# Optimization experiments

Measured on AMD Instinct MI355X. Metric: run time of the kernel, lower is better.

## Reference

```python
import jax, jax.numpy as jnp
import numpy as np

N = 250000   # num nodes
E = 250000   # num edges (tree: ~one parent per node)
D = 128      # embed_size
H = 256      # MLP hidden
HOPS = 3


def _mlp(x, w1, b1, w2, b2):
    # Sequential(Linear, ReLU, Linear, ReLU, Dropout(eval=identity))
    return jax.nn.relu(jnp.dot(jax.nn.relu(jnp.dot(x, w1) + b1), w2) + b2)


def _scatter_mean(src, idx, n):
    s = jax.ops.segment_sum(src, idx, num_segments=n)
    c = jax.ops.segment_sum(jnp.ones((src.shape[0],), src.dtype), idx, num_segments=n)
    return s / jnp.maximum(c, 1.0)[:, None]


def setup_inputs() -> dict:
    key = jax.random.key(0)
    ks = jax.random.split(key, 32)
    u = lambda k, shp: jax.random.uniform(k, shp, jnp.float32, -0.1, 0.1)
    inp = {
        "batch_token": jax.random.normal(ks[0], (N, D), jnp.float32),
        "self_idx_batch": jax.random.randint(ks[1], (E,), 0, N),
        "parent_idx_batch": jax.random.randint(ks[2], (E,), 0, N),
        "root_mask": (jax.random.uniform(ks[3], (N,)) < 0.01).astype(jnp.float32),
        "leaf_mask": (jax.random.uniform(ks[4], (N,)) < 0.3).astype(jnp.float32),
        "start_token": jax.random.normal(ks[5], (D,), jnp.float32),
        "end_token": jax.random.normal(ks[6], (D,), jnp.float32),
        # MLP_V: D -> H -> D
        "Vw1": u(ks[7], (D, H)), "Vb1": u(ks[8], (H,)), "Vw2": u(ks[9], (H, D)), "Vb2": u(ks[10], (D,)),
        # MLP_E: 1 -> H -> D
        "Ew1": u(ks[11], (1, H)), "Eb1": u(ks[12], (H,)), "Ew2": u(ks[13], (H, D)), "Eb2": u(ks[14], (D,)),
        # MLP_p: 3D -> H -> D
        "Pw1": u(ks[15], (3 * D, H)), "Pb1": u(ks[16], (H,)), "Pw2": u(ks[17], (H, D)), "Pb2": u(ks[18], (D,)),
        # MLP_c: 3D -> H -> D
        "Cw1": u(ks[19], (3 * D, H)), "Cb1": u(ks[20], (H,)), "Cw2": u(ks[21], (H, D)), "Cb2": u(ks[22], (D,)),
        # MLP_aggr: 3D -> H -> D
        "Aw1": u(ks[23], (3 * D, H)), "Ab1": u(ks[24], (H,)), "Aw2": u(ks[25], (H, D)), "Ab2": u(ks[26], (D,)),
    }
    return inp


def reference(batch_token, self_idx_batch, parent_idx_batch, root_mask, leaf_mask,
              start_token, end_token,
              Vw1, Vb1, Vw2, Vb2,
              Ew1, Eb1, Ew2, Eb2,
              Pw1, Pb1, Pw2, Pb2,
              Cw1, Cb1, Cw2, Cb2,
              Aw1, Ab1, Aw2, Ab2):
    n = batch_token.shape[0]
    edge_in = _mlp(jnp.ones((1, 1), batch_token.dtype), Ew1, Eb1, Ew2, Eb2)   # [1,D]
    edge_out = _mlp(jnp.zeros((1, 1), batch_token.dtype), Ew1, Eb1, Ew2, Eb2)  # [1,D]
    e = self_idx_batch.shape[0]
    edge_in = jnp.broadcast_to(edge_in, (e, edge_in.shape[1]))
    edge_out = jnp.broadcast_to(edge_out, (e, edge_out.shape[1]))

    hidden = _mlp(batch_token, Vw1, Vb1, Vw2, Vb2)  # [N,D]
    for _ in range(HOPS):
        node_self = hidden[self_idx_batch]      # [E,D] gather
        node_parent = hidden[parent_idx_batch]  # [E,D] gather
        inp_parent = jnp.concatenate([node_parent, node_self, edge_out], axis=-1)  # [E,3D]
        inp_child = jnp.concatenate([node_self, node_parent, edge_in], axis=-1)    # [E,3D]
        S_p = _mlp(inp_parent, Pw1, Pb1, Pw2, Pb2)
        S_c = _mlp(inp_child, Cw1, Cb1, Cw2, Cb2)
        S_p = _scatter_mean(S_p, self_idx_batch, n)
        S_c = _scatter_mean(S_c, parent_idx_batch, n)
        S_p = S_p + root_mask[:, None] * start_token
        S_c = S_c + leaf_mask[:, None] * end_token
        x_aggr = jnp.concatenate([hidden, S_p, S_c], axis=-1)  # [N,3D]
        hidden = hidden + _mlp(x_aggr, Aw1, Ab1, Aw2, Ab2)
    return hidden
```

## Files before the change

### kernel.cpp

```cpp
#include <hip/hip_runtime.h>

typedef __attribute__((ext_vector_type(8))) short short8;
typedef __attribute__((ext_vector_type(4))) float f32x4;

#define DD 128
#define HH 256

__device__ __forceinline__ unsigned short f2bf(float f) {
  unsigned int u = __float_as_uint(f);
  u += 0x7fffu + ((u >> 16) & 1u);
  return (unsigned short)(u >> 16);
}
__device__ __forceinline__ float bf2f(unsigned short s) {
  return __uint_as_float(((unsigned int)s) << 16);
}
__device__ __forceinline__ f32x4 mfma16(short8 a, short8 b, f32x4 c) {
  return __builtin_amdgcn_mfma_f32_16x16x32_bf16(a, b, c, 0, 0, 0);
}

__global__ void wconv(const float* __restrict__ src, unsigned short* __restrict__ dst,
                      int K, int Nout, int kswap) {
  int id = blockIdx.x * 256 + threadIdx.x;
  if (id >= K * Nout) return;
  int n = id / K, k = id - n * K;
  int ks = k + kswap; if (ks >= K) ks -= K;
  dst[n * K + k] = f2bf(src[(size_t)ks * Nout + n]);
}

__global__ void prep_bias(const float* __restrict__ Ew1, const float* __restrict__ Eb1,
                          const float* __restrict__ Ew2, const float* __restrict__ Eb2,
                          const float* __restrict__ Pw1, const float* __restrict__ Pb1,
                          const float* __restrict__ Cw1, const float* __restrict__ Cb1,
                          float* __restrict__ b1P, float* __restrict__ b1C) {
  __shared__ float h1[HH], h0[HH], ein[DD], eout[DD];
  int t = threadIdx.x;
  h1[t] = fmaxf(Ew1[t] + Eb1[t], 0.f);
  h0[t] = fmaxf(Eb1[t], 0.f);
  __syncthreads();
  if (t < DD) {
    float s1 = Eb2[t], s0 = Eb2[t];
    for (int j = 0; j < HH; ++j) { s1 += h1[j] * Ew2[j * DD + t]; s0 += h0[j] * Ew2[j * DD + t]; }
    ein[t]  = fmaxf(s1, 0.f);
    eout[t] = fmaxf(s0, 0.f);
  }
  __syncthreads();
  float bp = Pb1[t], bc = Cb1[t];
  for (int d = 0; d < DD; ++d) {
    bp += eout[d] * Pw1[(size_t)(256 + d) * HH + t];
    bc += ein[d]  * Cw1[(size_t)(256 + d) * HH + t];
  }
  b1P[t] = bp; b1C[t] = bc;
}

__global__ void count_k(const int* __restrict__ selfI, const int* __restrict__ parI,
                        int* degP, int* degC, int E) {
  int id = blockIdx.x * 256 + threadIdx.x;
  if (id < E) { atomicAdd(&degP[selfI[id]], 1); atomicAdd(&degC[parI[id]], 1); }
}

__global__ void scan1(const int* __restrict__ src, int* __restrict__ dst,
                      int* __restrict__ part, int n) {
  __shared__ int sh[256];
  int t = threadIdx.x;
  int base = blockIdx.x * 1024 + t * 4;
  int v0 = base + 0 < n ? src[base + 0] : 0;
  int v1 = base + 1 < n ? src[base + 1] : 0;
  int v2 = base + 2 < n ? src[base + 2] : 0;
  int v3 = base + 3 < n ? src[base + 3] : 0;
  int tsum = v0 + v1 + v2 + v3;
  sh[t] = tsum;
  __syncthreads();
  for (int off = 1; off < 256; off <<= 1) {
    int y = (t >= off) ? sh[t - off] : 0;
    __syncthreads();
    if (t >= off) sh[t] += y;
    __syncthreads();
  }
  int ex = sh[t] - tsum;
  if (base + 0 < n) dst[base + 0] = ex;
  if (base + 1 < n) dst[base + 1] = ex + v0;
  if (base + 2 < n) dst[base + 2] = ex + v0 + v1;
  if (base + 3 < n) dst[base + 3] = ex + v0 + v1 + v2;
  if (t == 255) part[blockIdx.x] = sh[255];
}

__global__ void scan2(int* __restrict__ part, int m) {
  __shared__ int sh[256];
  int t = threadIdx.x;
  int carry = 0;
  for (int base = 0; base < m; base += 256) {
    int v = (base + t < m) ? part[base + t] : 0;
    sh[t] = v;
    __syncthreads();
    for (int off = 1; off < 256; off <<= 1) {
      int y = (t >= off) ? sh[t - off] : 0;
      __syncthreads();
      if (t >= off) sh[t] += y;
      __syncthreads();
    }
    if (base + t < m) part[base + t] = carry + sh[t] - v;
    int tot = sh[255];
    __syncthreads();
    carry += tot;
  }
}

__global__ void scan3(int* __restrict__ dst, const int* __restrict__ part, int n) {
  int i = blockIdx.x * 256 + threadIdx.x;
  if (i < n) dst[i] += part[i >> 10];
}

__global__ void copy2(const int* __restrict__ a, int* __restrict__ b,
                      const int* __restrict__ c, int* __restrict__ d, int n) {
  int i = blockIdx.x * 256 + threadIdx.x;
  if (i < n) { b[i] = a[i]; d[i] = c[i]; }
}

__global__ void pos_k(const int* __restrict__ selfI, const int* __restrict__ parI,
                      int* curP, int* curC, int* posP, int* posC, int E) {
  int e = blockIdx.x * 256 + threadIdx.x;
  if (e < E) {
    posP[e] = atomicAdd(&curP[selfI[e]], 1);
    posC[e] = atomicAdd(&curC[parI[e]], 1);
  }
}

__global__ __launch_bounds__(256) void v_kernel(
    const float* __restrict__ x, const unsigned short* __restrict__ W1t,
    const unsigned short* __restrict__ W2t, const float* __restrict__ b1,
    const float* __restrict__ b2, float* __restrict__ hidden, int n) {
  __shared__ __align__(16) unsigned short A[64 * 136];
  __shared__ __align__(16) unsigned short O1[64 * 264];
  int t = threadIdx.x;
  int w = t >> 6, lane = t & 63, ln = lane & 15, quad = lane >> 4, qo = quad * 8;
  long tile0 = (long)blockIdx.x * 64;
  int rl = t >> 2, part = t & 3;
  long gr = tile0 + rl;
  const float* src = x + (size_t)(gr < n ? gr : 0) * DD + part * 32;
  unsigned short* arow = A + rl * 136 + part * 32;
#pragma unroll
  for (int i = 0; i < 8; ++i) {
    float4 v = *(const float4*)(src + i * 4);
    *(ushort4*)(arow + i * 4) = make_ushort4(f2bf(v.x), f2bf(v.y), f2bf(v.z), f2bf(v.w));
  }
  const unsigned short* aRow = A + (w * 16 + ln) * 136;
  f32x4 zero4 = {0.f, 0.f, 0.f, 0.f};
  f32x4 acc1[16];
#pragma unroll
  for (int nt = 0; nt < 16; ++nt) acc1[nt] = zero4;
#pragma unroll
  for (int kt = 0; kt < 4; ++kt) {
    short8 a = *(const short8*)(aRow + kt * 32 + qo);
#pragma unroll
    for (int nt = 0; nt < 16; ++nt) {
      short8 b = *(const short8*)(W1t + (size_t)(nt * 16 + ln) * 128 + kt * 32 + qo);
      acc1[nt] = mfma16(a, b, acc1[nt]);
    }
  }
#pragma unroll
  for (int nt = 0; nt < 16; ++nt) {
    float bb = b1[nt * 16 + ln];
#pragma unroll
    for (int r = 0; r < 4; ++r)
      O1[(w * 16 + quad * 4 + r) * 264 + nt * 16 + ln] = f2bf(fmaxf(acc1[nt][r] + bb, 0.f));
  }
  const unsigned short* oRow = O1 + (w * 16 + ln) * 264;
  f32x4 acc2[8];
#pragma unroll
  for (int nt = 0; nt < 8; ++nt) acc2[nt] = zero4;
#pragma unroll
  for (int kt = 0; kt < 8; ++kt) {
    short8 a = *(const short8*)(oRow + kt * 32 + qo);
#pragma unroll
    for (int nt = 0; nt < 8; ++nt) {
      short8 b = *(const short8*)(W2t + (size_t)(nt * 16 + ln) * 256 + kt * 32 + qo);
      acc2[nt] = mfma16(a, b, acc2[nt]);
    }
  }
#pragma unroll
  for (int nt = 0; nt < 8; ++nt) {
    float bb = b2[nt * 16 + ln];
#pragma unroll
    for (int r = 0; r < 4; ++r) {
      long gr2 = tile0 + w * 16 + quad * 4 + r;
      if (gr2 < n) hidden[gr2 * DD + nt * 16 + ln] = fmaxf(acc2[nt][r] + bb, 0.f);
    }
  }
}

__global__ __launch_bounds__(512, 4) void edge_kernel(
    const float* __restrict__ hidden, const int* __restrict__ selfI, const int* __restrict__ parI,
    const int* __restrict__ posP, const int* __restrict__ posC,
    const unsigned short* __restrict__ Pw1t, const unsigned short* __restrict__ Pw2t,
    const unsigned short* __restrict__ Cw1t, const unsigned short* __restrict__ Cw2t,
    const float* __restrict__ b1P, const float* __restrict__ b1C,
    const float* __restrict__ b2P, const float* __restrict__ b2C,
    unsigned short* __restrict__ SpE, unsigned short* __restrict__ ScE, int E) {
  __shared__ __align__(16) unsigned short A[64 * 264];
  __shared__ __align__(16) unsigned short O1[64 * 264];
  int t = threadIdx.x;
  int w = t >> 6, lane = t & 63, ln = lane & 15, quad = lane >> 4, qo = quad * 8;
  long tile0 = (long)blockIdx.x * 64;
  int rl = t >> 3, part = t & 7;
  long ge = tile0 + rl;
  bool vrow = ge < E;
  int si = vrow ? selfI[ge] : 0;
  int pi = vrow ? parI[ge] : 0;
  const float* src = (part < 4) ? (hidden + (size_t)si * DD + part * 32)
                                : (hidden + (size_t)pi * DD + (part - 4) * 32);
  unsigned short* dstA = A + rl * 264 + part * 32;
#pragma unroll
  for (int i = 0; i < 8; ++i) {
    float4 v = *(const float4*)(src + i * 4);
    *(ushort4*)(dstA + i * 4) = make_ushort4(f2bf(v.x), f2bf(v.y), f2bf(v.z), f2bf(v.w));
  }
  __syncthreads();

  for (int mlp = 0; mlp < 2; ++mlp) {
    const unsigned short* W1t = mlp ? Cw1t : Pw1t;
    const unsigned short* W2t = mlp ? Cw2t : Pw2t;
    const float* b1 = mlp ? b1C : b1P;
    const float* b2 = mlp ? b2C : b2P;
    unsigned short* Sout = mlp ? ScE : SpE;
    const int* pos = mlp ? posC : posP;
    f32x4 acc[4][2];
#pragma unroll
    for (int m = 0; m < 4; ++m) {
      acc[m][0] = {0.f, 0.f, 0.f, 0.f}; acc[m][1] = {0.f, 0.f, 0.f, 0.f};
    }
#pragma unroll
    for (int kt = 0; kt < 8; ++kt) {
      short8 a[4];
#pragma unroll
      for (int m = 0; m < 4; ++m)
        a[m] = *(const short8*)(A + (m * 16 + ln) * 264 + kt * 32 + qo);
#pragma unroll
      for (int nn = 0; nn < 2; ++nn) {
        short8 b = *(const short8*)(W1t + (size_t)(w * 32 + nn * 16 + ln) * 256 + kt * 32 + qo);
#pragma unroll
        for (int m = 0; m < 4; ++m) acc[m][nn] = mfma16(a[m], b, acc[m][nn]);
      }
    }
#pragma unroll
    for (int nn = 0; nn < 2; ++nn) {
      int col = w * 32 + nn * 16 + ln;
      float bb = b1[col];
#pragma unroll
      for (int m = 0; m < 4; ++m)
#pragma unroll
        for (int r = 0; r < 4; ++r)
          O1[(m * 16 + quad * 4 + r) * 264 + col] = f2bf(fmaxf(acc[m][nn][r] + bb, 0.f));
    }
    __syncthreads();
    f32x4 acc2[4];
#pragma unroll
    for (int m = 0; m < 4; ++m) acc2[m] = {0.f, 0.f, 0.f, 0.f};
#pragma unroll
    for (int kt = 0; kt < 8; ++kt) {
      short8 b = *(const short8*)(W2t + (size_t)(w * 16 + ln) * 256 + kt * 32 + qo);
#pragma unroll
      for (int m = 0; m < 4; ++m) {
        short8 a = *(const short8*)(O1 + (m * 16 + ln) * 264 + kt * 32 + qo);
        acc2[m] = mfma16(a, b, acc2[m]);
      }
    }
    __syncthreads();
    {
      int col = w * 16 + ln;
      float bb = b2[col];
#pragma unroll
      for (int m = 0; m < 4; ++m)
#pragma unroll
        for (int r = 0; r < 4; ++r)
          O1[(m * 16 + quad * 4 + r) * 264 + col] = f2bf(fmaxf(acc2[m][r] + bb, 0.f));
    }
    __syncthreads();
    if (vrow) {
      int dpos = pos[ge];
      const unsigned short* srow = O1 + rl * 264 + part * 16;
      ushort4* dst = (ushort4*)(Sout + (size_t)dpos * DD + part * 16);
#pragma unroll
      for (int i = 0; i < 4; ++i) dst[i] = *(const ushort4*)(srow + i * 4);
    }
    __syncthreads();
  }
}

__global__ __launch_bounds__(512, 4) void node_kernel(
    float* __restrict__ hidden,
    const unsigned short* __restrict__ SpE, const unsigned short* __restrict__ ScE,
    const int* __restrict__ offP, const int* __restrict__ degP,
    const int* __restrict__ offC, const int* __restrict__ degC,
    const float* __restrict__ rootM, const float* __restrict__ leafM,
    const float* __restrict__ startT, const float* __restrict__ endT,
    const unsigned short* __restrict__ W1t, const unsigned short* __restrict__ W2t,
    const float* __restrict__ b1, const float* __restrict__ b2, int n) {
  __shared__ __align__(16) unsigned short A[64 * 392];
  int t = threadIdx.x;
  int w = t >> 6, lane = t & 63, ln = lane & 15, quad = lane >> 4, qo = quad * 8;
  long tile0 = (long)blockIdx.x * 64;
  int rl = t >> 3, part = t & 7;
  int c0 = part * 16;
  long gr = tile0 + rl;
  long g = (gr < n) ? gr : 0;
  unsigned short* arow = A + rl * 392;
  {
    const float* hrow = hidden + (size_t)g * DD + c0;
#pragma unroll
    for (int i = 0; i < 4; ++i) {
      float4 h = *(const float4*)(hrow + i * 4);
      *(ushort4*)(arow + c0 + i * 4) = make_ushort4(f2bf(h.x), f2bf(h.y), f2bf(h.z), f2bf(h.w));
    }
  }
  {
    int off = offP[g], dg = degP[g];
    float s[16];
#pragma unroll
    for (int i = 0; i < 16; ++i) s[i] = 0.f;
    for (int j = 0; j < dg; ++j) {
      const unsigned short* rr = SpE + (size_t)(off + j) * DD + c0;
#pragma unroll
      for (int i = 0; i < 4; ++i) {
        ushort4 u = *(const ushort4*)(rr + i * 4);
        s[i * 4 + 0] += bf2f(u.x); s[i * 4 + 1] += bf2f(u.y);
        s[i * 4 + 2] += bf2f(u.z); s[i * 4 + 3] += bf2f(u.w);
      }
    }
    float ip = 1.f / fmaxf((float)dg, 1.f);
    float rm = rootM[g];
#pragma unroll
    for (int i = 0; i < 4; ++i) {
      float4 st = *(const float4*)(startT + c0 + i * 4);
      *(ushort4*)(arow + 128 + c0 + i * 4) = make_ushort4(
          f2bf(s[i * 4 + 0] * ip + rm * st.x), f2bf(s[i * 4 + 1] * ip + rm * st.y),
          f2bf(s[i * 4 + 2] * ip + rm * st.z), f2bf(s[i * 4 + 3] * ip + rm * st.w));
    }
  }
  {
    int off = offC[g], dg = degC[g];
    float s[16];
#pragma unroll
    for (int i = 0; i < 16; ++i) s[i] = 0.f;
    for (int j = 0; j < dg; ++j) {
      const unsigned short* rr = ScE + (size_t)(off + j) * DD + c0;
#pragma unroll
      for (int i = 0; i < 4; ++i) {
        ushort4 u = *(const ushort4*)(rr + i * 4);
        s[i * 4 + 0] += bf2f(u.x); s[i * 4 + 1] += bf2f(u.y);
        s[i * 4 + 2] += bf2f(u.z); s[i * 4 + 3] += bf2f(u.w);
      }
    }
    float ic = 1.f / fmaxf((float)dg, 1.f);
    float lm = leafM[g];
#pragma unroll
    for (int i = 0; i < 4; ++i) {
      float4 et = *(const float4*)(endT + c0 + i * 4);
      *(ushort4*)(arow + 256 + c0 + i * 4) = make_ushort4(
          f2bf(s[i * 4 + 0] * ic + lm * et.x), f2bf(s[i * 4 + 1] * ic + lm * et.y),
          f2bf(s[i * 4 + 2] * ic + lm * et.z), f2bf(s[i * 4 + 3] * ic + lm * et.w));
    }
  }
  __syncthreads();
  f32x4 acc[4][2];
#pragma unroll
  for (int m = 0; m < 4; ++m) {
    acc[m][0] = {0.f, 0.f, 0.f, 0.f}; acc[m][1] = {0.f, 0.f, 0.f, 0.f};
  }
#pragma unroll
  for (int kt = 0; kt < 12; ++kt) {
    short8 a[4];
#pragma unroll
    for (int m = 0; m < 4; ++m)
      a[m] = *(const short8*)(A + (m * 16 + ln) * 392 + kt * 32 + qo);
#pragma unroll
    for (int nn = 0; nn < 2; ++nn) {
      short8 b = *(const short8*)(W1t + (size_t)(w * 32 + nn * 16 + ln) * 384 + kt * 32 + qo);
#pragma unroll
      for (int m = 0; m < 4; ++m) acc[m][nn] = mfma16(a[m], b, acc[m][nn]);
    }
  }
  __syncthreads();
#pragma unroll
  for (int nn = 0; nn < 2; ++nn) {
    int col = w * 32 + nn * 16 + ln;
    float bb = b1[col];
#pragma unroll
    for (int m = 0; m < 4; ++m)
#pragma unroll
      for (int r = 0; r < 4; ++r)
        A[(m * 16 + quad * 4 + r) * 392 + col] = f2bf(fmaxf(acc[m][nn][r] + bb, 0.f));
  }
  __syncthreads();
  f32x4 acc2[4];
#pragma unroll
  for (int m = 0; m < 4; ++m) acc2[m] = {0.f, 0.f, 0.f, 0.f};
#pragma unroll
  for (int kt = 0; kt < 8; ++kt) {
    short8 b = *(const short8*)(W2t + (size_t)(w * 16 + ln) * 256 + kt * 32 + qo);
#pragma unroll
    for (int m = 0; m < 4; ++m) {
      short8 a = *(const short8*)(A + (m * 16 + ln) * 392 + kt * 32 + qo);
      acc2[m] = mfma16(a, b, acc2[m]);
    }
  }
  __syncthreads();
  {
    int col = w * 16 + ln;
    float bb = b2[col];
#pragma unroll
    for (int m = 0; m < 4; ++m)
#pragma unroll
      for (int r = 0; r < 4; ++r)
        ((float*)(A + (size_t)(m * 16 + quad * 4 + r) * 392))[col] =
            fmaxf(acc2[m][r] + bb, 0.f);
  }
  __syncthreads();
  if (gr < n) {
    const float* F = (const float*)(A + (size_t)rl * 392);
    float* hrow = hidden + (size_t)gr * DD + c0;
#pragma unroll
    for (int i = 0; i < 4; ++i) {
      float4 v = *(const float4*)(F + c0 + i * 4);
      float4 h = *(const float4*)(hrow + i * 4);
      h.x += v.x; h.y += v.y; h.z += v.z; h.w += v.w;
      *(float4*)(hrow + i * 4) = h;
    }
  }
}

extern "C" void kernel_launch(void* const* d_in, const int* in_sizes, int n_in,
                              void* d_out, int out_size, void* d_ws, size_t ws_size,
                              hipStream_t stream) {
  const float* batch  = (const float*)d_in[0];
  const int*   selfI  = (const int*)d_in[1];
  const int*   parI   = (const int*)d_in[2];
  const float* rootM  = (const float*)d_in[3];
  const float* leafM  = (const float*)d_in[4];
  const float* startT = (const float*)d_in[5];
  const float* endT   = (const float*)d_in[6];
  const float* Vw1 = (const float*)d_in[7],  *Vb1 = (const float*)d_in[8];
  const float* Vw2 = (const float*)d_in[9],  *Vb2 = (const float*)d_in[10];
  const float* Ew1 = (const float*)d_in[11], *Eb1 = (const float*)d_in[12];
  const float* Ew2 = (const float*)d_in[13], *Eb2 = (const float*)d_in[14];
  const float* Pw1 = (const float*)d_in[15], *Pb1 = (const float*)d_in[16];
  const float* Pw2 = (const float*)d_in[17], *Pb2 = (const float*)d_in[18];
  const float* Cw1 = (const float*)d_in[19], *Cb1 = (const float*)d_in[20];
  const float* Cw2 = (const float*)d_in[21], *Cb2 = (const float*)d_in[22];
  const float* Aw1 = (const float*)d_in[23], *Ab1 = (const float*)d_in[24];
  const float* Aw2 = (const float*)d_in[25], *Ab2 = (const float*)d_in[26];

  const int N = in_sizes[3];
  const int E = in_sizes[1];
  float* out = (float*)d_out;

  char* p = (char*)d_ws;
  auto nxt = [&](size_t sz) { char* r = p; p += (sz + 255) & ~(size_t)255; return r; };
  unsigned short* SpE = (unsigned short*)nxt((size_t)E * DD * 2);
  unsigned short* ScE = (unsigned short*)nxt((size_t)E * DD * 2);
  int* degP = (int*)nxt((size_t)N * 4);
  int* degC = (int*)nxt((size_t)N * 4);
  int* offP = (int*)nxt((size_t)N * 4);
  int* offC = (int*)nxt((size_t)N * 4);
  int* curP = (int*)nxt((size_t)N * 4);
  int* curC = (int*)nxt((size_t)N * 4);
  int* posP = (int*)nxt((size_t)E * 4);
  int* posC = (int*)nxt((size_t)E * 4);
  int* partA = (int*)nxt(4096);
  int* partB = (int*)nxt(4096);
  unsigned short* Vw1t = (unsigned short*)nxt((size_t)128 * 256 * 2);
  unsigned short* Vw2t = (unsigned short*)nxt((size_t)256 * 128 * 2);
  unsigned short* Pw1t = (unsigned short*)nxt((size_t)256 * 256 * 2);
  unsigned short* Pw2t = (unsigned short*)nxt((size_t)256 * 128 * 2);
  unsigned short* Cw1t = (unsigned short*)nxt((size_t)256 * 256 * 2);
  unsigned short* Cw2t = (unsigned short*)nxt((size_t)256 * 128 * 2);
  unsigned short* Aw1t = (unsigned short*)nxt((size_t)384 * 256 * 2);
  unsigned short* Aw2t = (unsigned short*)nxt((size_t)256 * 128 * 2);
  float* b1P = (float*)nxt(256 * 4);
  float* b1C = (float*)nxt(256 * 4);

  hipMemsetAsync(degP, 0, (size_t)N * 4, stream);
  hipMemsetAsync(degC, 0, (size_t)N * 4, stream);

  auto blk = [](int total) { return dim3((total + 255) / 256); };
  wconv<<<blk(128 * 256), 256, 0, stream>>>(Vw1, Vw1t, 128, 256, 0);
  wconv<<<blk(256 * 128), 256, 0, stream>>>(Vw2, Vw2t, 256, 128, 0);
  wconv<<<blk(256 * 256), 256, 0, stream>>>(Pw1, Pw1t, 256, 256, 128);
  wconv<<<blk(256 * 128), 256, 0, stream>>>(Pw2, Pw2t, 256, 128, 0);
  wconv<<<blk(256 * 256), 256, 0, stream>>>(Cw1, Cw1t, 256, 256, 0);
  wconv<<<blk(256 * 128), 256, 0, stream>>>(Cw2, Cw2t, 256, 128, 0);
  wconv<<<blk(384 * 256), 256, 0, stream>>>(Aw1, Aw1t, 384, 256, 0);
  wconv<<<blk(256 * 128), 256, 0, stream>>>(Aw2, Aw2t, 256, 128, 0);

  prep_bias<<<1, 256, 0, stream>>>(Ew1, Eb1, Ew2, Eb2, Pw1, Pb1, Cw1, Cb1, b1P, b1C);
  count_k<<<blk(E), 256, 0, stream>>>(selfI, parI, degP, degC, E);

  int NB = (N + 1023) / 1024;
  scan1<<<NB, 256, 0, stream>>>(degP, offP, partA, N);
  scan1<<<NB, 256, 0, stream>>>(degC, offC, partB, N);
  scan2<<<1, 256, 0, stream>>>(partA, NB);
  scan2<<<1, 256, 0, stream>>>(partB, NB);
  scan3<<<blk(N), 256, 0, stream>>>(offP, partA, N);
  scan3<<<blk(N), 256, 0, stream>>>(offC, partB, N);
  copy2<<<blk(N), 256, 0, stream>>>(offP, curP, offC, curC, N);
  pos_k<<<blk(E), 256, 0, stream>>>(selfI, parI, curP, curC, posP, posC, E);

  dim3 gN((N + 63) / 64), gE((E + 63) / 64);
  v_kernel<<<gN, 256, 0, stream>>>(batch, Vw1t, Vw2t, Vb1, Vb2, out, N);

  for (int hop = 0; hop < 3; ++hop) {
    edge_kernel<<<gE, 512, 0, stream>>>(out, selfI, parI, posP, posC,
                                        Pw1t, Pw2t, Cw1t, Cw2t, b1P, b1C, Pb2, Cb2,
                                        SpE, ScE, E);
    node_kernel<<<gN, 512, 0, stream>>>(out, SpE, ScE, offP, degP, offC, degC,
                                        rootM, leafM, startT, endT,
                                        Aw1t, Aw2t, Ab1, Ab2, N);
  }
}
```

Measured before the change: 1.954 ms.

## Retile V MLP to 512 threads and share A-fragment loads across P/C first layers

The initial vertex MLP kernel moves from 4 waves (each owning 16 rows with all output columns) to 8 waves that split output columns across all 64 rows, matching the edge kernel's layout. It also adds a missing sync after the LDS staging. In the edge kernel, the first-layer GEMMs of the parent and child MLPs are computed in one K loop, so each A fragment read from LDS feeds both weight sets. This raises accumulator register pressure (16 f32x4 live), which may reduce occupancy under the 512,4 launch bounds.

```diff
diff --git a/kernel.cpp b/kernel.cpp
--- a/kernel.cpp
+++ b/kernel.cpp
@@ -125,7 +125,7 @@
   }
 }
 
-__global__ __launch_bounds__(256) void v_kernel(
+__global__ __launch_bounds__(512, 4) void v_kernel(
     const float* __restrict__ x, const unsigned short* __restrict__ W1t,
     const unsigned short* __restrict__ W2t, const float* __restrict__ b1,
     const float* __restrict__ b2, float* __restrict__ hidden, int n) {
@@ -134,57 +134,68 @@
   int t = threadIdx.x;
   int w = t >> 6, lane = t & 63, ln = lane & 15, quad = lane >> 4, qo = quad * 8;
   long tile0 = (long)blockIdx.x * 64;
-  int rl = t >> 2, part = t & 3;
+  int rl = t >> 3, part = t & 7;
+  int c0 = part * 16;
   long gr = tile0 + rl;
-  const float* src = x + (size_t)(gr < n ? gr : 0) * DD + part * 32;
-  unsigned short* arow = A + rl * 136 + part * 32;
-#pragma unroll
-  for (int i = 0; i < 8; ++i) {
+  const float* src = x + (size_t)(gr < n ? gr : 0) * DD + c0;
+  unsigned short* arow = A + rl * 136 + c0;
+#pragma unroll
+  for (int i = 0; i < 4; ++i) {
     float4 v = *(const float4*)(src + i * 4);
     *(ushort4*)(arow + i * 4) = make_ushort4(f2bf(v.x), f2bf(v.y), f2bf(v.z), f2bf(v.w));
   }
-  const unsigned short* aRow = A + (w * 16 + ln) * 136;
-  f32x4 zero4 = {0.f, 0.f, 0.f, 0.f};
-  f32x4 acc1[16];
-#pragma unroll
-  for (int nt = 0; nt < 16; ++nt) acc1[nt] = zero4;
+  __syncthreads();
+  f32x4 acc[4][2];
+#pragma unroll
+  for (int m = 0; m < 4; ++m) {
+    acc[m][0] = {0.f, 0.f, 0.f, 0.f}; acc[m][1] = {0.f, 0.f, 0.f, 0.f};
+  }
 #pragma unroll
   for (int kt = 0; kt < 4; ++kt) {
-    short8 a = *(const short8*)(aRow + kt * 32 + qo);
-#pragma unroll
-    for (int nt = 0; nt < 16; ++nt) {
-      short8 b = *(const short8*)(W1t + (size_t)(nt * 16 + ln) * 128 + kt * 32 + qo);
-      acc1[nt] = mfma16(a, b, acc1[nt]);
-    }
-  }
-#pragma unroll
-  for (int nt = 0; nt < 16; ++nt) {
-    float bb = b1[nt * 16 + ln];
-#pragma unroll
-    for (int r = 0; r < 4; ++r)
-      O1[(w * 16 + quad * 4 + r) * 264 + nt * 16 + ln] = f2bf(fmaxf(acc1[nt][r] + bb, 0.f));
-  }
-  const unsigned short* oRow = O1 + (w * 16 + ln) * 264;
-  f32x4 acc2[8];
-#pragma unroll
-  for (int nt = 0; nt < 8; ++nt) acc2[nt] = zero4;
+    short8 a[4];
+#pragma unroll
+    for (int m = 0; m < 4; ++m)
+      a[m] = *(const short8*)(A + (m * 16 + ln) * 136 + kt * 32 + qo);
+#pragma unroll
+    for (int nn = 0; nn < 2; ++nn) {
+      short8 b = *(const short8*)(W1t + (size_t)(w * 32 + nn * 16 + ln) * 128 + kt * 32 + qo);
+#pragma unroll
+      for (int m = 0; m < 4; ++m) acc[m][nn] = mfma16(a[m], b, acc[m][nn]);
+    }
+  }
+#pragma unroll
+  for (int nn = 0; nn < 2; ++nn) {
+    int col = w * 32 + nn * 16 + ln;
+    float bb = b1[col];
+#pragma unroll
+    for (int m = 0; m < 4; ++m)
+#pragma unroll
+      for (int r = 0; r < 4; ++r)
+        O1[(m * 16 + quad * 4 + r) * 264 + col] = f2bf(fmaxf(acc[m][nn][r] + bb, 0.f));
+  }
+  __syncthreads();
+  f32x4 acc2[4];
+#pragma unroll
+  for (int m = 0; m < 4; ++m) acc2[m] = {0.f, 0.f, 0.f, 0.f};
 #pragma unroll
   for (int kt = 0; kt < 8; ++kt) {
-    short8 a = *(const short8*)(oRow + kt * 32 + qo);
-#pragma unroll
-    for (int nt = 0; nt < 8; ++nt) {
-      short8 b = *(const short8*)(W2t + (size_t)(nt * 16 + ln) * 256 + kt * 32 + qo);
-      acc2[nt] = mfma16(a, b, acc2[nt]);
-    }
-  }
-#pragma unroll
-  for (int nt = 0; nt < 8; ++nt) {
-    float bb = b2[nt * 16 + ln];
-#pragma unroll
-    for (int r = 0; r < 4; ++r) {
-      long gr2 = tile0 + w * 16 + quad * 4 + r;
-      if (gr2 < n) hidden[gr2 * DD + nt * 16 + ln] = fmaxf(acc2[nt][r] + bb, 0.f);
-    }
+    short8 b = *(const short8*)(W2t + (size_t)(w * 16 + ln) * 256 + kt * 32 + qo);
+#pragma unroll
+    for (int m = 0; m < 4; ++m) {
+      short8 a = *(const short8*)(O1 + (m * 16 + ln) * 264 + kt * 32 + qo);
+      acc2[m] = mfma16(a, b, acc2[m]);
+    }
+  }
+  {
+    int col = w * 16 + ln;
+    float bb = b2[col];
+#pragma unroll
+    for (int m = 0; m < 4; ++m)
+#pragma unroll
+      for (int r = 0; r < 4; ++r) {
+        long gr2 = tile0 + m * 16 + quad * 4 + r;
+        if (gr2 < n) hidden[gr2 * DD + col] = fmaxf(acc2[m][r] + bb, 0.f);
+      }
   }
 }
 
@@ -216,31 +227,38 @@
   }
   __syncthreads();
 
+  f32x4 accP[4][2], accC[4][2];
+#pragma unroll
+  for (int m = 0; m < 4; ++m) {
+    accP[m][0] = {0.f, 0.f, 0.f, 0.f}; accP[m][1] = {0.f, 0.f, 0.f, 0.f};
+    accC[m][0] = {0.f, 0.f, 0.f, 0.f}; accC[m][1] = {0.f, 0.f, 0.f, 0.f};
+  }
+#pragma unroll
+  for (int kt = 0; kt < 8; ++kt) {
+    short8 a[4];
+#pragma unroll
+    for (int m = 0; m < 4; ++m)
+      a[m] = *(const short8*)(A + (m * 16 + ln) * 264 + kt * 32 + qo);
+#pragma unroll
+    for (int nn = 0; nn < 2; ++nn) {
+      short8 bp = *(const short8*)(Pw1t + (size_t)(w * 32 + nn * 16 + ln) * 256 + kt * 32 + qo);
+      short8 bc = *(const short8*)(Cw1t + (size_t)(w * 32 + nn * 16 + ln) * 256 + kt * 32 + qo);
+#pragma unroll
+      for (int m = 0; m < 4; ++m) {
+        accP[m][nn] = mfma16(a[m], bp, accP[m][nn]);
+        accC[m][nn] = mfma16(a[m], bc, accC[m][nn]);
+      }
+    }
+  }
+  __syncthreads();
+
+#pragma unroll
   for (int mlp = 0; mlp < 2; ++mlp) {
-    const unsigned short* W1t = mlp ? Cw1t : Pw1t;
     const unsigned short* W2t = mlp ? Cw2t : Pw2t;
     const float* b1 = mlp ? b1C : b1P;
     const float* b2 = mlp ? b2C : b2P;
     unsigned short* Sout = mlp ? ScE : SpE;
     const int* pos = mlp ? posC : posP;
-    f32x4 acc[4][2];
-#pragma unroll
-    for (int m = 0; m < 4; ++m) {
-      acc[m][0] = {0.f, 0.f, 0.f, 0.f}; acc[m][1] = {0.f, 0.f, 0.f, 0.f};
-    }
-#pragma unroll
-    for (int kt = 0; kt < 8; ++kt) {
-      short8 a[4];
-#pragma unroll
-      for (int m = 0; m < 4; ++m)
-        a[m] = *(const short8*)(A + (m * 16 + ln) * 264 + kt * 32 + qo);
-#pragma unroll
-      for (int nn = 0; nn < 2; ++nn) {
-        short8 b = *(const short8*)(W1t + (size_t)(w * 32 + nn * 16 + ln) * 256 + kt * 32 + qo);
-#pragma unroll
-        for (int m = 0; m < 4; ++m) acc[m][nn] = mfma16(a[m], b, acc[m][nn]);
-      }
-    }
 #pragma unroll
     for (int nn = 0; nn < 2; ++nn) {
       int col = w * 32 + nn * 16 + ln;
@@ -248,8 +266,10 @@
 #pragma unroll
       for (int m = 0; m < 4; ++m)
 #pragma unroll
-        for (int r = 0; r < 4; ++r)
-          O1[(m * 16 + quad * 4 + r) * 264 + col] = f2bf(fmaxf(acc[m][nn][r] + bb, 0.f));
+        for (int r = 0; r < 4; ++r) {
+          float v = mlp ? accC[m][nn][r] : accP[m][nn][r];
+          O1[(m * 16 + quad * 4 + r) * 264 + col] = f2bf(fmaxf(v + bb, 0.f));
+        }
     }
     __syncthreads();
     f32x4 acc2[4];
@@ -505,7 +525,7 @@
   pos_k<<<blk(E), 256, 0, stream>>>(selfI, parI, curP, curC, posP, posC, E);
 
   dim3 gN((N + 63) / 64), gE((E + 63) / 64);
-  v_kernel<<<gN, 256, 0, stream>>>(batch, Vw1t, Vw2t, Vb1, Vb2, out, N);
+  v_kernel<<<gN, 512, 0, stream>>>(batch, Vw1t, Vw2t, Vb1, Vb2, out, N);
 
   for (int hop = 0; hop < 3; ++hop) {
     edge_kernel<<<gE, 512, 0, stream>>>(out, selfI, parI, posP, posC,
```

Measured after the change: 1.831 ms. -6.3%, faster.
